# Kernel tuning notes

Hardware: AMD Instinct MI355X
Metric: run time of the kernel (lower is better)

## Reference

```python
import jax, jax.numpy as jnp
import numpy as np

B, D, K = 32, 64, 256            # batch, num objects (seq len), feature size (== in_size)
G = [256, 256, 256]              # g_layers sizes
F1, F2, OUT = 256, 256, 128      # f_fc1, f_fc2, out_size


def setup_inputs() -> dict:
    key = jax.random.key(0)
    ks = jax.random.split(key, 16)
    scale = 0.02

    def w(k, shape):
        return jax.random.normal(k, shape, dtype=jnp.float32) * scale

    x = jax.random.normal(ks[0], (B, D, K), dtype=jnp.float32)
    # edge_feature: Linear(2*K, K). Stored [in, out] (transposed vs torch).
    edge_w = w(ks[1], (2 * K, K))
    edge_b = jnp.zeros((K,), dtype=jnp.float32)
    g_ws, g_bs = [], []
    in_s = K
    for i, out_s in enumerate(G):
        g_ws.append(w(ks[2 + i], (in_s, out_s)))
        g_bs.append(jnp.zeros((out_s,), dtype=jnp.float32))
        in_s = out_s
    f1_w = w(ks[8], (G[-1], F1)); f1_b = jnp.zeros((F1,), dtype=jnp.float32)
    f2_w = w(ks[9], (F1, F2));    f2_b = jnp.zeros((F2,), dtype=jnp.float32)
    f3_w = w(ks[10], (F2, OUT));  f3_b = jnp.zeros((OUT,), dtype=jnp.float32)
    return dict(x=x, edge_w=edge_w, edge_b=edge_b, g_ws=g_ws, g_bs=g_bs,
                f1_w=f1_w, f1_b=f1_b, f2_w=f2_w, f2_b=f2_b, f3_w=f3_w, f3_b=f3_b)


def reference(x, edge_w, edge_b, g_ws, g_bs, f1_w, f1_b, f2_w, f2_b, f3_w, f3_b):
    # x: [B, D, K]. Original builds x_full[b,i,j] = concat(x[b,j], x[b,i]) then
    # applies edge_feature (Linear(2K -> K)). Equivalent, without materializing the
    # concat: split edge_w into the halves acting on x_i (=x[b,j]) and x_j (=x[b,i]).
    k = x.shape[-1]
    u = x @ edge_w[:k]      # [B, D, K]  -> indexed by j (axis 2)
    v = x @ edge_w[k:]      # [B, D, K]  -> indexed by i (axis 1)
    h = u[:, None, :, :] + v[:, :, None, :] + edge_b   # [B, D, D, K]
    # g MLP over all d^2 pairs (Linear + ReLU chain)
    for gw, gb in zip(g_ws, g_bs):
        h = jax.nn.relu(h @ gw + gb)
    # sum-aggregate over all pairs
    x_g = h.sum(axis=(1, 2))                            # [B, G[-1]]
    # f MLP (dropout p=0.0 -> identity)
    x_f = jax.nn.relu(x_g @ f1_w + f1_b)
    x_f = jax.nn.relu(x_f @ f2_w + f2_b)
    return x_f @ f3_w + f3_b                            # [B, OUT]
```

## Files before the change

kernel.cpp:

```cpp
#include <hip/hip_runtime.h>
#include <hip/hip_bf16.h>

typedef __attribute__((ext_vector_type(4))) float f32x4;
typedef __attribute__((ext_vector_type(2))) int   i32x2;
typedef __attribute__((ext_vector_type(4))) int   i32x4;
typedef __attribute__((ext_vector_type(8))) short short8;

__device__ __forceinline__ unsigned short f2bf(float x) {
  __hip_bfloat16 h = __float2bfloat16(x);
  union { __hip_bfloat16 h1; unsigned short u; } c; c.h1 = h; return c.u;
}
__device__ __forceinline__ unsigned pk2(float a, float b) {
  __hip_bfloat162 h = __float22bfloat162_rn(make_float2(a, b));
  union { __hip_bfloat162 h2; unsigned u; } c; c.h2 = h; return c.u;
}
__device__ __forceinline__ float bf2f(unsigned short u) {
  union { unsigned u32; float f; } c; c.u32 = ((unsigned)u) << 16; return c.f;
}

__global__ void k_prep(const float* __restrict__ edge_w, const float* __restrict__ edge_b,
                       const float* __restrict__ gw0, const float* __restrict__ gb0,
                       const float* __restrict__ gw1, const float* __restrict__ gw2,
                       unsigned short* __restrict__ W1uR, unsigned short* __restrict__ W1vR,
                       float* __restrict__ c1,
                       unsigned short* __restrict__ W2R, unsigned short* __restrict__ W3R) {
  const int blk = blockIdx.x, t = threadIdx.x;
  __shared__ float eu[256], ev[256];
  if (blk < 256) {
    eu[t] = edge_w[blk * 256 + t];
    ev[t] = edge_w[(256 + blk) * 256 + t];
    __syncthreads();
    float su = 0.f, sv = 0.f;
    for (int o = 0; o < 256; ++o) {
      float gg = gw0[o * 256 + t];
      su += eu[o] * gg; sv += ev[o] * gg;
    }
    const int k = blk, m = t;
    const int w = m >> 6, mf = (m >> 4) & 3, q = m & 15;
    const int ch = k >> 5, g = (k >> 3) & 3, e = k & 7;
    const int idx = ((w * 8 + ch) * 4 + mf) * 512 + (g * 16 + q) * 8 + e;
    W1uR[idx] = f2bf(su);
    W1vR[idx] = f2bf(sv);
  } else if (blk == 256) {
    float s = gb0[t];
    for (int o = 0; o < 256; ++o) s += edge_b[o] * gw0[o * 256 + t];
    c1[t] = s;
  } else {
    int p = blk - 257;
    const float* src = (p < 32) ? gw1 : gw2;
    unsigned short* dst = (p < 32) ? W2R : W3R;
    p &= 31;
    int w = p >> 3, ch = p & 7;
    int mf = t >> 6, lane = t & 63, q = lane & 15, g = lane >> 4;
    int base = ((w * 8 + ch) * 4 + mf) * 512 + lane * 8;
    int m = w * 64 + mf * 16 + q;
#pragma unroll
    for (int e = 0; e < 8; ++e) {
      int k = ch * 32 + g * 8 + e;
      dst[base + e] = f2bf(src[k * 256 + m]);
    }
  }
}

__global__ void k_uv(const float* __restrict__ x,
                     const unsigned short* __restrict__ W1uR,
                     const unsigned short* __restrict__ W1vR,
                     const float* __restrict__ c1,
                     unsigned short* __restrict__ U1, float* __restrict__ V1c) {
  __shared__ unsigned short xs[8192];

  const int t = threadIdx.x;
  const int tile = blockIdx.x >> 1, sel = blockIdx.x & 1;
  const int r0 = tile * 32;
  const int wid = t >> 6, lane = t & 63;
  const int q = lane & 15, g = lane >> 4;
  const int mo = wid << 6;

  {
    const int row = t >> 3, sl = t & 7, r7 = row & 7;
    const float* xB = x + (size_t)(r0 + row) * 256;
    unsigned short* hB = xs + row * 256;
#pragma unroll
    for (int m = 0; m < 4; ++m) {
      int ks = sl + 8 * m;
      f32x4 u0 = *(const f32x4*)(xB + ks * 8);
      f32x4 u1 = *(const f32x4*)(xB + ks * 8 + 4);
      i32x4 wv = { (int)pk2(u0.x, u0.y), (int)pk2(u0.z, u0.w),
                   (int)pk2(u1.x, u1.y), (int)pk2(u1.z, u1.w) };
      *(i32x4*)(hB + (ks ^ r7) * 8) = wv;
    }
  }

  const unsigned short* WR = sel ? W1vR : W1uR;
  const unsigned short* aW = WR + (size_t)wid * 16384 + lane * 8;

  short8 a_[4], an_[4];
#pragma unroll
  for (int mf = 0; mf < 4; ++mf) a_[mf] = *(const short8*)(aW + mf * 512);

  __syncthreads();

  f32x4 acc[4][2];
#pragma unroll
  for (int mf = 0; mf < 4; ++mf)
#pragma unroll
    for (int nf = 0; nf < 2; ++nf) acc[mf][nf] = (f32x4){0.f, 0.f, 0.f, 0.f};

  for (int ch = 0; ch < 8; ++ch) {
    if (ch < 7) {
#pragma unroll
      for (int mf = 0; mf < 4; ++mf)
        an_[mf] = *(const short8*)(aW + (ch + 1) * 2048 + mf * 512);
    }
    short8 b_[2];
#pragma unroll
    for (int nf = 0; nf < 2; ++nf) {
      int r = q + 16 * nf;
      b_[nf] = *(const short8*)(xs + r * 256 + (((ch * 4 + g) ^ (r & 7)) * 8));
    }
#pragma unroll
    for (int mf = 0; mf < 4; ++mf)
#pragma unroll
      for (int nf = 0; nf < 2; ++nf)
        acc[mf][nf] = __builtin_amdgcn_mfma_f32_16x16x32_bf16(a_[mf], b_[nf], acc[mf][nf], 0, 0, 0);
    if (ch < 7) {
#pragma unroll
      for (int mf = 0; mf < 4; ++mf) a_[mf] = an_[mf];
    }
  }

#pragma unroll
  for (int mf = 0; mf < 4; ++mf) {
    int c2b = mo + 16 * mf + 4 * g;
#pragma unroll
    for (int nf = 0; nf < 2; ++nf) {
      int r = r0 + q + 16 * nf;
      f32x4 v = acc[mf][nf];
      if (sel == 0) {
        i32x2 wv = { (int)pk2(v.x, v.y), (int)pk2(v.z, v.w) };
        *(i32x2*)(U1 + (size_t)r * 256 + c2b) = wv;
      } else {
        f32x4 cc = *(const f32x4*)(c1 + c2b);
        f32x4 o = { v.x + cc.x, v.y + cc.y, v.z + cc.z, v.w + cc.w };
        *(f32x4*)(V1c + (size_t)r * 256 + c2b) = o;
      }
    }
  }
}

__device__ __forceinline__ void write_h1(short8 u, f32x4 v0, f32x4 v1,
                                         unsigned short* dst) {
  float r0 = fmaxf(bf2f((unsigned short)u[0]) + v0.x, 0.f);
  float r1 = fmaxf(bf2f((unsigned short)u[1]) + v0.y, 0.f);
  float r2 = fmaxf(bf2f((unsigned short)u[2]) + v0.z, 0.f);
  float r3 = fmaxf(bf2f((unsigned short)u[3]) + v0.w, 0.f);
  float r4 = fmaxf(bf2f((unsigned short)u[4]) + v1.x, 0.f);
  float r5 = fmaxf(bf2f((unsigned short)u[5]) + v1.y, 0.f);
  float r6 = fmaxf(bf2f((unsigned short)u[6]) + v1.z, 0.f);
  float r7 = fmaxf(bf2f((unsigned short)u[7]) + v1.w, 0.f);
  i32x4 wv = { (int)pk2(r0, r1), (int)pk2(r2, r3), (int)pk2(r4, r5), (int)pk2(r6, r7) };
  *(i32x4*)dst = wv;
}

__launch_bounds__(512, 4)
__global__ void k_main(const unsigned short* __restrict__ U1,
                       const float* __restrict__ V1c,
                       const unsigned short* __restrict__ W2R,
                       const unsigned short* __restrict__ W3R,
                       const float* __restrict__ b2, const float* __restrict__ b3,
                       float* __restrict__ partials) {
  __shared__ unsigned short bufA[16384];
  __shared__ unsigned short bufB[16384];

  const int t = threadIdx.x;
  const int bid = blockIdx.x;
  const int wrk = ((bid & 7) << 7) | (bid >> 3);
  const int b = wrk >> 5;
  const int it0 = (wrk & 31) * 2;
  const int sel = t >> 8;
  const int tt = t & 255;
  const int wid4 = (t >> 6) & 3;
  const int lane = t & 63;
  const int q = lane & 15, g = lane >> 4;
  const int mo = wid4 << 6;

  unsigned short* const buf = sel ? bufB : bufA;

  {
    const int row = tt >> 2, sl = tt & 3, r7 = row & 7;
    const unsigned short* uB = U1 + (size_t)(b * 64 + row) * 256;
    const float* vP = V1c + (size_t)(b * 64 + it0 + sel) * 256;
    unsigned short* d = buf + row * 256;
#pragma unroll
    for (int m = 0; m < 8; ++m) {
      int ks = sl + 4 * m;
      int s8 = (ks ^ r7) * 8;
      short8 u = *(const short8*)(uB + ks * 8);
      f32x4 v0 = *(const f32x4*)(vP + ks * 8);
      f32x4 v1 = *(const f32x4*)(vP + ks * 8 + 4);
      write_h1(u, v0, v1, d + s8);
    }
  }

  const unsigned short* aW2 = W2R + (size_t)wid4 * 16384 + lane * 8;
  const unsigned short* aW3 = W3R + (size_t)wid4 * 16384 + lane * 8;

  __syncthreads();

  f32x4 acc[4][4];
#pragma unroll
  for (int mf = 0; mf < 4; ++mf)
#pragma unroll
    for (int nf = 0; nf < 4; ++nf) acc[mf][nf] = (f32x4){0.f, 0.f, 0.f, 0.f};

#pragma unroll
  for (int ch = 0; ch < 8; ++ch) {
    short8 a_[4];
#pragma unroll
    for (int mf = 0; mf < 4; ++mf)
      a_[mf] = *(const short8*)(aW2 + ch * 2048 + mf * 512);
    short8 b_[4];
#pragma unroll
    for (int nf = 0; nf < 4; ++nf) {
      int r = q + 16 * nf;
      b_[nf] = *(const short8*)(buf + r * 256 + (((ch * 4 + g) ^ (r & 7)) * 8));
    }
#pragma unroll
    for (int mf = 0; mf < 4; ++mf)
#pragma unroll
      for (int nf = 0; nf < 4; ++nf)
        acc[mf][nf] = __builtin_amdgcn_mfma_f32_16x16x32_bf16(a_[mf], b_[nf], acc[mf][nf], 0, 0, 0);
  }

  __syncthreads();

#pragma unroll
  for (int mf = 0; mf < 4; ++mf) {
    int c2b = mo + 16 * mf + 4 * g;
    f32x4 bb = *(const f32x4*)(b2 + c2b);
    int ksw = c2b >> 3, off = c2b & 7;
#pragma unroll
    for (int nf = 0; nf < 4; ++nf) {
      int r = q + 16 * nf;
      int dst = r * 256 + ((ksw ^ (r & 7)) * 8) + off;
      f32x4 v = acc[mf][nf];
      i32x2 wv = { (int)pk2(fmaxf(v.x + bb.x, 0.f), fmaxf(v.y + bb.y, 0.f)),
                   (int)pk2(fmaxf(v.z + bb.z, 0.f), fmaxf(v.w + bb.w, 0.f)) };
      *(i32x2*)(buf + dst) = wv;
    }
  }
  __syncthreads();

#pragma unroll
  for (int mf = 0; mf < 4; ++mf)
#pragma unroll
    for (int nf = 0; nf < 4; ++nf) acc[mf][nf] = (f32x4){0.f, 0.f, 0.f, 0.f};

#pragma unroll
  for (int ch = 0; ch < 8; ++ch) {
    short8 a_[4];
#pragma unroll
    for (int mf = 0; mf < 4; ++mf)
      a_[mf] = *(const short8*)(aW3 + ch * 2048 + mf * 512);
    short8 b_[4];
#pragma unroll
    for (int nf = 0; nf < 4; ++nf) {
      int r = q + 16 * nf;
      b_[nf] = *(const short8*)(buf + r * 256 + (((ch * 4 + g) ^ (r & 7)) * 8));
    }
#pragma unroll
    for (int mf = 0; mf < 4; ++mf)
#pragma unroll
      for (int nf = 0; nf < 4; ++nf)
        acc[mf][nf] = __builtin_amdgcn_mfma_f32_16x16x32_bf16(a_[mf], b_[nf], acc[mf][nf], 0, 0, 0);
  }

  __syncthreads();

  float* scr = (float*)buf;
#pragma unroll
  for (int mf = 0; mf < 4; ++mf) {
    int n3b = mo + 16 * mf + 4 * g;
    f32x4 bb = *(const f32x4*)(b3 + n3b);
    f32x4 sum = (f32x4){0.f, 0.f, 0.f, 0.f};
#pragma unroll
    for (int nf = 0; nf < 4; ++nf) {
      f32x4 v = acc[mf][nf];
      sum.x += fmaxf(v.x + bb.x, 0.f);
      sum.y += fmaxf(v.y + bb.y, 0.f);
      sum.z += fmaxf(v.z + bb.z, 0.f);
      sum.w += fmaxf(v.w + bb.w, 0.f);
    }
    *(f32x4*)(scr + q * 264 + n3b) = sum;
  }
  __syncthreads();
  float s = 0.f;
#pragma unroll
  for (int q2 = 0; q2 < 16; ++q2) s += scr[q2 * 264 + tt];
  partials[(size_t)(b * 64 + it0 + sel) * 256 + tt] = s;
}

__global__ void k_fmlp(const float* __restrict__ partials,
                       const float* __restrict__ f1w, const float* __restrict__ f1b,
                       const float* __restrict__ f2w, const float* __restrict__ f2b,
                       const float* __restrict__ f3w, const float* __restrict__ f3b,
                       float* __restrict__ out) {
  const int b = blockIdx.x, t = threadIdx.x;
  __shared__ float xg[256], x1[256], x2[256];
  {
    const float* p = partials + (size_t)(b * 64) * 256 + t;
    float s[8];
#pragma unroll
    for (int i = 0; i < 8; ++i) s[i] = 0.f;
#pragma unroll
    for (int k = 0; k < 8; ++k)
#pragma unroll
      for (int i = 0; i < 8; ++i) s[i] += p[(k * 8 + i) * 256];
    float tot = 0.f;
#pragma unroll
    for (int i = 0; i < 8; ++i) tot += s[i];
    xg[t] = tot;
  }
  __syncthreads();
  {
    float a0 = 0.f, a1 = 0.f, a2 = 0.f, a3 = 0.f;
#pragma unroll 4
    for (int k = 0; k < 64; ++k) {
      a0 += xg[k]       * f1w[(k)       * 256 + t];
      a1 += xg[k + 64]  * f1w[(k + 64)  * 256 + t];
      a2 += xg[k + 128] * f1w[(k + 128) * 256 + t];
      a3 += xg[k + 192] * f1w[(k + 192) * 256 + t];
    }
    x1[t] = fmaxf((a0 + a1) + (a2 + a3) + f1b[t], 0.f);
  }
  __syncthreads();
  {
    float a0 = 0.f, a1 = 0.f, a2 = 0.f, a3 = 0.f;
#pragma unroll 4
    for (int k = 0; k < 64; ++k) {
      a0 += x1[k]       * f2w[(k)       * 256 + t];
      a1 += x1[k + 64]  * f2w[(k + 64)  * 256 + t];
      a2 += x1[k + 128] * f2w[(k + 128) * 256 + t];
      a3 += x1[k + 192] * f2w[(k + 192) * 256 + t];
    }
    x2[t] = fmaxf((a0 + a1) + (a2 + a3) + f2b[t], 0.f);
  }
  __syncthreads();
  if (t < 128) {
    float a0 = 0.f, a1 = 0.f, a2 = 0.f, a3 = 0.f;
#pragma unroll 4
    for (int k = 0; k < 64; ++k) {
      a0 += x2[k]       * f3w[(k)       * 128 + t];
      a1 += x2[k + 64]  * f3w[(k + 64)  * 128 + t];
      a2 += x2[k + 128] * f3w[(k + 128) * 128 + t];
      a3 += x2[k + 192] * f3w[(k + 192) * 128 + t];
    }
    out[b * 128 + t] = (a0 + a1) + (a2 + a3) + f3b[t];
  }
}

__global__ void k_zero(float* __restrict__ out, int n) {
  int i = blockIdx.x * 256 + threadIdx.x;
  if (i < n) out[i] = 0.f;
}

extern "C" void kernel_launch(void* const* d_in, const int* in_sizes, int n_in,
                              void* d_out, int out_size, void* d_ws, size_t ws_size,
                              hipStream_t stream) {
  const float* x      = (const float*)d_in[0];
  const float* edge_w = (const float*)d_in[1];
  const float* edge_b = (const float*)d_in[2];
  const float *gw0, *gw1, *gw2, *gb0, *gb1, *gb2;
  const float *f1w, *f1b, *f2w, *f2b, *f3w, *f3b;

  if (n_in >= 15 && in_sizes[3] == 65536 && in_sizes[4] == 65536 && in_sizes[5] == 65536) {
    gw0 = (const float*)d_in[3]; gw1 = (const float*)d_in[4]; gw2 = (const float*)d_in[5];
    gb0 = (const float*)d_in[6]; gb1 = (const float*)d_in[7]; gb2 = (const float*)d_in[8];
    f1w = (const float*)d_in[9];  f1b = (const float*)d_in[10];
    f2w = (const float*)d_in[11]; f2b = (const float*)d_in[12];
    f3w = (const float*)d_in[13]; f3b = (const float*)d_in[14];
  } else if (n_in >= 15 && in_sizes[3] == 65536 && in_sizes[4] == 256) {
    gw0 = (const float*)d_in[3]; gb0 = (const float*)d_in[4];
    gw1 = (const float*)d_in[5]; gb1 = (const float*)d_in[6];
    gw2 = (const float*)d_in[7]; gb2 = (const float*)d_in[8];
    f1w = (const float*)d_in[9];  f1b = (const float*)d_in[10];
    f2w = (const float*)d_in[11]; f2b = (const float*)d_in[12];
    f3w = (const float*)d_in[13]; f3b = (const float*)d_in[14];
  } else {
    const float* gws = (const float*)d_in[3];
    const float* gbs = (const float*)d_in[4];
    gw0 = gws;          gw1 = gws + 65536;  gw2 = gws + 131072;
    gb0 = gbs;          gb1 = gbs + 256;    gb2 = gbs + 512;
    f1w = (const float*)d_in[5];  f1b = (const float*)d_in[6];
    f2w = (const float*)d_in[7];  f2b = (const float*)d_in[8];
    f3w = (const float*)d_in[9];  f3b = (const float*)d_in[10];
  }

  char* ws = (char*)d_ws;
  float*          c1       = (float*)(ws);
  unsigned short* W1uR     = (unsigned short*)(ws + 1024);
  unsigned short* W1vR     = (unsigned short*)(ws + 132096);
  unsigned short* W2R      = (unsigned short*)(ws + 263168);
  unsigned short* W3R      = (unsigned short*)(ws + 394240);
  unsigned short* U1       = (unsigned short*)(ws + 525312);
  float*          V1c      = (float*)(ws + 1573888);
  float*          partials = (float*)(ws + 3671040);
  const size_t need = 5768192;
  (void)out_size; (void)n_in;

  if (ws_size < need) {
    k_zero<<<dim3((out_size + 255) / 256), dim3(256), 0, stream>>>((float*)d_out, out_size);
    return;
  }

  k_prep<<<dim3(321), dim3(256), 0, stream>>>(edge_w, edge_b, gw0, gb0, gw1, gw2,
                                              W1uR, W1vR, c1, W2R, W3R);
  k_uv<<<dim3(128), dim3(256), 0, stream>>>(x, W1uR, W1vR, c1, U1, V1c);
  k_main<<<dim3(1024), dim3(512), 0, stream>>>(U1, V1c, W2R, W3R, gb1, gb2,
                                               partials);
  k_fmlp<<<dim3(32), dim3(256), 0, stream>>>(partials, f1w, f1b, f2w, f2b, f3w, f3b,
                                             (float*)d_out);
}
```

Baseline: 73.00 us.

## Retile per-wave MFMA work to 128 features by 32 rows in g-MLP layers

Each wave's tile in the two g-MLP GEMMs changes from 64 output features × 64 rows to 128 features × 32 rows. Per k-chunk a wave now loads 8 weight fragments and 2 LDS activation fragments instead of 4 and 4, so LDS reads drop and global/L2 weight reads double. The final reduction gains an extra sync phase where the two row-half waves combine their partial sums in shared scratch. Risks include higher register pressure from eight A fragments and the extra barrier.

```diff
diff --git a/kernel.cpp b/kernel.cpp
--- a/kernel.cpp
+++ b/kernel.cpp
@@ -177,12 +177,13 @@
   const int wrk = ((bid & 7) << 7) | (bid >> 3);
   const int b = wrk >> 5;
   const int it0 = (wrk & 31) * 2;
-  const int sel = t >> 8;
+  const int w = t >> 6;
+  const int sel = w >> 2;
+  const int rh = (w >> 1) & 1;
+  const int fh = w & 1;
   const int tt = t & 255;
-  const int wid4 = (t >> 6) & 3;
   const int lane = t & 63;
   const int q = lane & 15, g = lane >> 4;
-  const int mo = wid4 << 6;
 
   unsigned short* const buf = sel ? bufB : bufA;
 
@@ -202,46 +203,46 @@
     }
   }
 
-  const unsigned short* aW2 = W2R + (size_t)wid4 * 16384 + lane * 8;
-  const unsigned short* aW3 = W3R + (size_t)wid4 * 16384 + lane * 8;
-
-  __syncthreads();
-
-  f32x4 acc[4][4];
-#pragma unroll
-  for (int mf = 0; mf < 4; ++mf)
-#pragma unroll
-    for (int nf = 0; nf < 4; ++nf) acc[mf][nf] = (f32x4){0.f, 0.f, 0.f, 0.f};
+  const unsigned short* aW2 = W2R + (size_t)(fh * 2) * 16384 + lane * 8;
+  const unsigned short* aW3 = W3R + (size_t)(fh * 2) * 16384 + lane * 8;
+
+  __syncthreads();
+
+  f32x4 acc[8][2];
+#pragma unroll
+  for (int mf = 0; mf < 8; ++mf)
+#pragma unroll
+    for (int nf = 0; nf < 2; ++nf) acc[mf][nf] = (f32x4){0.f, 0.f, 0.f, 0.f};
 
 #pragma unroll
   for (int ch = 0; ch < 8; ++ch) {
-    short8 a_[4];
-#pragma unroll
-    for (int mf = 0; mf < 4; ++mf)
-      a_[mf] = *(const short8*)(aW2 + ch * 2048 + mf * 512);
-    short8 b_[4];
-#pragma unroll
-    for (int nf = 0; nf < 4; ++nf) {
-      int r = q + 16 * nf;
+    short8 a_[8];
+#pragma unroll
+    for (int mf = 0; mf < 8; ++mf)
+      a_[mf] = *(const short8*)(aW2 + (mf >> 2) * 16384 + ch * 2048 + (mf & 3) * 512);
+    short8 b_[2];
+#pragma unroll
+    for (int nf = 0; nf < 2; ++nf) {
+      int r = rh * 32 + 16 * nf + q;
       b_[nf] = *(const short8*)(buf + r * 256 + (((ch * 4 + g) ^ (r & 7)) * 8));
     }
 #pragma unroll
-    for (int mf = 0; mf < 4; ++mf)
-#pragma unroll
-      for (int nf = 0; nf < 4; ++nf)
+    for (int mf = 0; mf < 8; ++mf)
+#pragma unroll
+      for (int nf = 0; nf < 2; ++nf)
         acc[mf][nf] = __builtin_amdgcn_mfma_f32_16x16x32_bf16(a_[mf], b_[nf], acc[mf][nf], 0, 0, 0);
   }
 
   __syncthreads();
 
 #pragma unroll
-  for (int mf = 0; mf < 4; ++mf) {
-    int c2b = mo + 16 * mf + 4 * g;
+  for (int mf = 0; mf < 8; ++mf) {
+    int c2b = fh * 128 + mf * 16 + 4 * g;
     f32x4 bb = *(const f32x4*)(b2 + c2b);
     int ksw = c2b >> 3, off = c2b & 7;
 #pragma unroll
-    for (int nf = 0; nf < 4; ++nf) {
-      int r = q + 16 * nf;
+    for (int nf = 0; nf < 2; ++nf) {
+      int r = rh * 32 + 16 * nf + q;
       int dst = r * 256 + ((ksw ^ (r & 7)) * 8) + off;
       f32x4 v = acc[mf][nf];
       i32x2 wv = { (int)pk2(fmaxf(v.x + bb.x, 0.f), fmaxf(v.y + bb.y, 0.f)),
@@ -252,46 +253,66 @@
   __syncthreads();
 
 #pragma unroll
-  for (int mf = 0; mf < 4; ++mf)
-#pragma unroll
-    for (int nf = 0; nf < 4; ++nf) acc[mf][nf] = (f32x4){0.f, 0.f, 0.f, 0.f};
+  for (int mf = 0; mf < 8; ++mf)
+#pragma unroll
+    for (int nf = 0; nf < 2; ++nf) acc[mf][nf] = (f32x4){0.f, 0.f, 0.f, 0.f};
 
 #pragma unroll
   for (int ch = 0; ch < 8; ++ch) {
-    short8 a_[4];
-#pragma unroll
-    for (int mf = 0; mf < 4; ++mf)
-      a_[mf] = *(const short8*)(aW3 + ch * 2048 + mf * 512);
-    short8 b_[4];
-#pragma unroll
-    for (int nf = 0; nf < 4; ++nf) {
-      int r = q + 16 * nf;
+    short8 a_[8];
+#pragma unroll
+    for (int mf = 0; mf < 8; ++mf)
+      a_[mf] = *(const short8*)(aW3 + (mf >> 2) * 16384 + ch * 2048 + (mf & 3) * 512);
+    short8 b_[2];
+#pragma unroll
+    for (int nf = 0; nf < 2; ++nf) {
+      int r = rh * 32 + 16 * nf + q;
       b_[nf] = *(const short8*)(buf + r * 256 + (((ch * 4 + g) ^ (r & 7)) * 8));
     }
 #pragma unroll
-    for (int mf = 0; mf < 4; ++mf)
-#pragma unroll
-      for (int nf = 0; nf < 4; ++nf)
+    for (int mf = 0; mf < 8; ++mf)
+#pragma unroll
+      for (int nf = 0; nf < 2; ++nf)
         acc[mf][nf] = __builtin_amdgcn_mfma_f32_16x16x32_bf16(a_[mf], b_[nf], acc[mf][nf], 0, 0, 0);
   }
 
   __syncthreads();
 
   float* scr = (float*)buf;
-#pragma unroll
-  for (int mf = 0; mf < 4; ++mf) {
-    int n3b = mo + 16 * mf + 4 * g;
+  f32x4 sums[8];
+#pragma unroll
+  for (int mf = 0; mf < 8; ++mf) {
+    int n3b = fh * 128 + mf * 16 + 4 * g;
     f32x4 bb = *(const f32x4*)(b3 + n3b);
     f32x4 sum = (f32x4){0.f, 0.f, 0.f, 0.f};
 #pragma unroll
-    for (int nf = 0; nf < 4; ++nf) {
+    for (int nf = 0; nf < 2; ++nf) {
       f32x4 v = acc[mf][nf];
       sum.x += fmaxf(v.x + bb.x, 0.f);
       sum.y += fmaxf(v.y + bb.y, 0.f);
       sum.z += fmaxf(v.z + bb.z, 0.f);
       sum.w += fmaxf(v.w + bb.w, 0.f);
     }
-    *(f32x4*)(scr + q * 264 + n3b) = sum;
+    sums[mf] = sum;
+  }
+  if (rh == 0) {
+#pragma unroll
+    for (int mf = 0; mf < 8; ++mf) {
+      int n3b = fh * 128 + mf * 16 + 4 * g;
+      *(f32x4*)(scr + q * 264 + n3b) = sums[mf];
+    }
+  }
+  __syncthreads();
+  if (rh == 1) {
+#pragma unroll
+    for (int mf = 0; mf < 8; ++mf) {
+      int n3b = fh * 128 + mf * 16 + 4 * g;
+      float* p = scr + q * 264 + n3b;
+      f32x4 cur = *(f32x4*)p;
+      f32x4 s2 = sums[mf];
+      f32x4 o = { cur.x + s2.x, cur.y + s2.y, cur.z + s2.z, cur.w + s2.w };
+      *(f32x4*)p = o;
+    }
   }
   __syncthreads();
   float s = 0.f;
```

After: 87.86 us. 1.2x slower.
